# Kernel optimization log

Hardware: AMD Instinct MI355X
Metric: run time of the kernel (lower is better)

## Reference

```python
import jax, jax.numpy as jnp
import numpy as np

N_HEAD = 12

def setup_inputs() -> dict:
    key = jax.random.key(0)
    ks = jax.random.split(key, 3)
    B, T, D = 4, 2048, 768
    x = jax.random.normal(ks[0], (B, T, D), dtype=jnp.float32)
    W_qkv = jax.random.normal(ks[1], (D, 3 * D), dtype=jnp.float32) * (1.0 / np.sqrt(D))
    b_qkv = jnp.zeros((3 * D,), dtype=jnp.float32)
    W_o = jax.random.normal(ks[2], (D, D), dtype=jnp.float32) * (1.0 / np.sqrt(D))
    b_o = jnp.zeros((D,), dtype=jnp.float32)
    return {"x": x, "W_qkv": W_qkv, "b_qkv": b_qkv, "W_o": W_o, "b_o": b_o}


def reference(x, W_qkv, b_qkv, W_o, b_o):
    B, T, D = x.shape
    H = N_HEAD
    hd = D // H
    qkv = x @ W_qkv + b_qkv                      # [B,T,3D]
    q, k, v = jnp.split(qkv, 3, axis=-1)
    # [B,T,D] -> [B,H,T,hd]
    q = q.reshape(B, T, H, hd).transpose(0, 2, 1, 3)
    k = k.reshape(B, T, H, hd).transpose(0, 2, 1, 3)
    v = v.reshape(B, T, H, hd).transpose(0, 2, 1, 3)
    scale = 1.0 / np.sqrt(hd).astype(np.float32)
    scores = jnp.einsum('bhqd,bhkd->bhqk', q, k) * scale   # [B,H,T,T]
    causal = jnp.tril(jnp.ones((T, T), dtype=bool))
    scores = jnp.where(causal[None, None, :, :], scores, -jnp.inf)
    attn = jax.nn.softmax(scores, axis=-1)
    out = jnp.einsum('bhqk,bhkd->bhqd', attn, v)            # [B,H,T,hd]
    out = out.transpose(0, 2, 1, 3).reshape(B, T, D)
    return out @ W_o + b_o
```

## Files before the change

kernel.cpp:

```cpp
#include <hip/hip_runtime.h>
#include <hip/hip_bf16.h>

typedef __bf16 bf16_t;
typedef float f32x4 __attribute__((ext_vector_type(4)));
typedef bf16_t bf16x8 __attribute__((ext_vector_type(8)));
typedef bf16_t bf16x4 __attribute__((ext_vector_type(4)));

#define MFMA16(a, b, c) __builtin_amdgcn_mfma_f32_16x16x32_bf16(a, b, c, 0, 0, 0)

#define QSCALE 0.18033688011112042f

__device__ __forceinline__ void gl_lds16(const bf16_t* g, bf16_t* l) {
    __builtin_amdgcn_global_load_lds(
        (const __attribute__((address_space(1))) unsigned int*)g,
        (__attribute__((address_space(3))) unsigned int*)l, 16, 0, 0);
}

__device__ __forceinline__ float fexp2(float x) {
    float y;
    asm("v_exp_f32 %0, %1" : "=v"(y) : "v"(x));
    return y;
}

__global__ __launch_bounds__(256) void conv_x(const float* __restrict__ in,
                                              bf16_t* __restrict__ out, int n) {
    int i = (blockIdx.x * 256 + threadIdx.x) * 4;
    if (i >= n) return;
    float4 v = *(const float4*)(in + i);
    bf16x4 o = { (bf16_t)v.x, (bf16_t)v.y, (bf16_t)v.z, (bf16_t)v.w };
    *(bf16x4*)(out + i) = o;
}

__global__ __launch_bounds__(256) void conv_t(const float* __restrict__ in,
                                              bf16_t* __restrict__ out,
                                              int R, int C) {
    __shared__ float t[32][33];
    const int bx = blockIdx.x * 32;
    const int by = blockIdx.y * 32;
    const int tx = threadIdx.x & 31;
    const int ty = threadIdx.x >> 5;
#pragma unroll
    for (int i = 0; i < 4; i++)
        t[ty + i * 8][tx] = in[(size_t)(by + ty + i * 8) * C + bx + tx];
    __syncthreads();
#pragma unroll
    for (int i = 0; i < 4; i++)
        out[(size_t)(bx + ty + i * 8) * R + by + tx] = (bf16_t)t[tx][ty + i * 8];
}

__global__ __launch_bounds__(256) void vtrans(const bf16_t* __restrict__ Vp,
                                              bf16_t* __restrict__ Vt) {
    __shared__ __align__(16) bf16_t Ts[64 * 72];
    const int t0 = blockIdx.x * 64;
    const int bh = blockIdx.y;
    const int r  = threadIdx.x >> 2;
    const int cb = (threadIdx.x & 3) * 16;
    const bf16_t* src = Vp + (((size_t)bh * 2048 + t0 + r) << 6) + cb;
    *(bf16x8*)(Ts + r * 72 + cb)     = *(const bf16x8*)(src);
    *(bf16x8*)(Ts + r * 72 + cb + 8) = *(const bf16x8*)(src + 8);
    __syncthreads();
    const int f  = threadIdx.x >> 2;
    const int tb = (threadIdx.x & 3) * 16;
    bf16_t* dst = Vt + (((size_t)bh * 64 + f) << 11) + t0 + tb;
    bf16x8 a, b;
#pragma unroll
    for (int i = 0; i < 8; i++) a[i] = Ts[(tb + i) * 72 + f];
#pragma unroll
    for (int i = 0; i < 8; i++) b[i] = Ts[(tb + 8 + i) * 72 + f];
    *(bf16x8*)(dst)     = a;
    *(bf16x8*)(dst + 8) = b;
}

template <int EPI>
__global__ __launch_bounds__(256) void gemm_bt(
    const bf16_t* __restrict__ A, const bf16_t* __restrict__ Bt,
    const float* __restrict__ bias,
    void* __restrict__ O0v, bf16_t* __restrict__ O1, bf16_t* __restrict__ O2,
    int M, int N, int K)
{
    __shared__ __align__(16) bf16_t As[2][128 * 32];
    __shared__ __align__(16) bf16_t Bs[2][128 * 32];

    const int tid  = threadIdx.x;
    const int wid  = tid >> 6;
    const int lane = tid & 63;
    const int quad = lane >> 4;
    const int l15  = lane & 15;
    const int wm   = (wid >> 1) * 64;
    const int wn   = (wid & 1) * 64;

    const int mtiles = M >> 7;
    const int mtpx   = mtiles >> 3;
    const int bid    = blockIdx.x;
    const int xcd    = bid & 7;
    const int slot   = bid >> 3;
    const int m0     = (xcd * mtpx + (slot % mtpx)) << 7;
    const int n0     = (slot / mtpx) << 7;

    f32x4 acc[4][4];
#pragma unroll
    for (int i = 0; i < 4; i++)
#pragma unroll
        for (int j = 0; j < 4; j++) acc[i][j] = (f32x4){0.f, 0.f, 0.f, 0.f};

    const int srow = tid >> 2;
    const int scol = (tid & 3) * 8;
    const bf16_t* ag0 = A  + (size_t)(m0 + srow) * K + scol;
    const bf16_t* ag1 = A  + (size_t)(m0 + 64 + srow) * K + scol;
    const bf16_t* bg0 = Bt + (size_t)(n0 + srow) * K + scol;
    const bf16_t* bg1 = Bt + (size_t)(n0 + 64 + srow) * K + scol;

    auto prefetch = [&](int k0, int buf) {
        gl_lds16(ag0 + k0, As[buf] + tid * 8);
        gl_lds16(ag1 + k0, As[buf] + 2048 + tid * 8);
        gl_lds16(bg0 + k0, Bs[buf] + tid * 8);
        gl_lds16(bg1 + k0, Bs[buf] + 2048 + tid * 8);
    };

    const int niter = K >> 5;
    prefetch(0, 0);
    for (int i = 0; i < niter; i++) {
        __syncthreads();
        if (i + 1 < niter) prefetch((i + 1) << 5, (i + 1) & 1);
        const bf16_t* Ap = As[i & 1];
        const bf16_t* Bp = Bs[i & 1];

        bf16x8 af[4], bfr[4];
#pragma unroll
        for (int ii = 0; ii < 4; ii++)
            af[ii] = *(const bf16x8*)(Ap + (wm + ii * 16 + l15) * 32 + quad * 8);
#pragma unroll
        for (int j = 0; j < 4; j++)
            bfr[j] = *(const bf16x8*)(Bp + (wn + j * 16 + l15) * 32 + quad * 8);
#pragma unroll
        for (int ii = 0; ii < 4; ii++)
#pragma unroll
            for (int j = 0; j < 4; j++)
                acc[ii][j] = MFMA16(af[ii], bfr[j], acc[ii][j]);
    }

    if (EPI == 0) {
        const int sec = n0 / 768;
        const float scale = (sec == 0) ? QSCALE : 1.f;
        bf16_t* dst = (sec == 0) ? (bf16_t*)O0v : (sec == 1 ? O1 : O2);
#pragma unroll
        for (int i = 0; i < 4; i++) {
            const int mbase = m0 + wm + i * 16 + quad * 4;
#pragma unroll
            for (int j = 0; j < 4; j++) {
                const int n  = n0 + wn + j * 16 + l15;
                const float bv = bias[n];
                const int d    = n - sec * 768;
                const int h    = d >> 6;
                const int feat = d & 63;
#pragma unroll
                for (int r = 0; r < 4; r++) {
                    const int mm = mbase + r;
                    const int b  = mm >> 11;
                    const int tt = mm & 2047;
                    const int bh = b * 12 + h;
                    dst[(((size_t)bh * 2048 + tt) << 6) + feat] =
                        (bf16_t)((acc[i][j][r] + bv) * scale);
                }
            }
        }
    } else {
#pragma unroll
        for (int i = 0; i < 4; i++) {
            const int mbase = m0 + wm + i * 16 + quad * 4;
#pragma unroll
            for (int j = 0; j < 4; j++) {
                const int n  = n0 + wn + j * 16 + l15;
                const float bv = bias[n];
#pragma unroll
                for (int r = 0; r < 4; r++)
                    ((float*)O0v)[(size_t)(mbase + r) * N + n] = acc[i][j][r] + bv;
            }
        }
    }
}

__global__ __launch_bounds__(256) void attn_k(
    const bf16_t* __restrict__ Q, const bf16_t* __restrict__ Kb,
    const bf16_t* __restrict__ Vt,
    bf16_t* __restrict__ Op0, bf16_t* __restrict__ Op1,
    float* __restrict__ Lp0, float* __restrict__ Lp1)
{
    __shared__ __align__(16) bf16_t Ks[2 * 4096];
    __shared__ __align__(16) bf16_t Vs[2 * 4096];
    __shared__ __align__(16) bf16_t Ps[4 * 16 * 64];

    const int tid  = threadIdx.x;
    const int wid  = tid >> 6;
    const int lane = tid & 63;
    const int quad = lane >> 4;
    const int l15  = lane & 15;

    const int bid  = blockIdx.x;
    const int xcd  = bid & 7;
    const int slot = bid >> 3;
    const int bh   = xcd * 6 + (slot >> 5);
    const int px   = slot & 31;
    const int p    = px >> 1;
    const int hpar = px & 1;

    const bf16_t* Qb  = Q  + ((size_t)bh << 17);
    const bf16_t* Kbh = Kb + ((size_t)bh << 17);
    const bf16_t* Vbh = Vt + ((size_t)bh << 17);

    bf16_t* Pw = Ps + wid * 1024;
    const int swl = l15 & 7;
    bf16_t* pwr[4];
#pragma unroll
    for (int c = 0; c < 4; c++)
        pwr[c] = Pw + l15 * 64 + (((((c << 1) | (quad >> 1))) ^ swl) << 3) + ((quad & 1) << 2);
    const bf16_t* prd[2];
#pragma unroll
    for (int kk = 0; kk < 2; kk++)
        prd[kk] = Pw + l15 * 64 + ((((kk << 2) | quad) ^ swl) << 3);

    bf16_t* Op = hpar ? Op1 : Op0;
    float*  Lp = hpar ? Lp1 : Lp0;

    const bf16x8 ones = { (bf16_t)1.f, (bf16_t)1.f, (bf16_t)1.f, (bf16_t)1.f,
                          (bf16_t)1.f, (bf16_t)1.f, (bf16_t)1.f, (bf16_t)1.f };

    const int srow = tid >> 2;
    const int scol = (tid & 3) * 8;

    auto prefetch = [&](int j, int buf) {
        const int kv0 = j * 64;
        bf16_t* kd = Ks + buf * 4096 + tid * 8;
        bf16_t* vd = Vs + buf * 4096 + tid * 8;
#pragma unroll
        for (int c = 0; c < 2; c++) {
            gl_lds16(Kbh + (size_t)(kv0 + srow) * 64 + c * 32 + scol, kd + c * 2048);
            gl_lds16(Vbh + (size_t)srow * 2048 + kv0 + c * 32 + scol, vd + c * 2048);
        }
    };

#pragma unroll
    for (int half = 0; half < 2; half++) {
        const int qt = half == 0 ? (31 - p) : p;
        const int q0 = qt * 64;
        const int qg = q0 + wid * 16 + l15;

        bf16x8 qf[2];
        {
            const bf16_t* qp = Qb + ((size_t)qg << 6) + quad * 8;
            qf[0] = *(const bf16x8*)(qp);
            qf[1] = *(const bf16x8*)(qp + 32);
        }

        f32x4 lacc = (f32x4){0.f, 0.f, 0.f, 0.f};
        f32x4 oacc[4];
#pragma unroll
        for (int f = 0; f < 4; f++) oacc[f] = (f32x4){0.f, 0.f, 0.f, 0.f};

        const int cnt = (qt >= hpar) ? ((qt - hpar) >> 1) + 1 : 0;
        if (cnt > 0) prefetch(hpar, 0);

        for (int i = 0; i < cnt; i++) {
            const int j   = hpar + 2 * i;
            const int kv0 = j * 64;
            __syncthreads();
            if (i + 1 < cnt) prefetch(j + 2, (i + 1) & 1);
            const bf16_t* Kp = Ks + (i & 1) * 4096;
            const bf16_t* Vp = Vs + (i & 1) * 4096;

            f32x4 st[4];
#pragma unroll
            for (int c = 0; c < 4; c++) {
                st[c] = (f32x4){0.f, 0.f, 0.f, 0.f};
#pragma unroll
                for (int kk = 0; kk < 2; kk++) {
                    bf16x8 kf = *(const bf16x8*)(Kp + kk * 2048 + (c * 16 + l15) * 32 + quad * 8);
                    st[c] = MFMA16(kf, qf[kk], st[c]);
                }
            }

            if (j == qt) {
                const int kvb = kv0 + quad * 4;
#pragma unroll
                for (int c = 0; c < 4; c++)
#pragma unroll
                    for (int r = 0; r < 4; r++)
                        if (kvb + c * 16 + r > qg) st[c][r] = -3e38f;
            }

#pragma unroll
            for (int c = 0; c < 4; c++) {
                bf16x4 pk = { (bf16_t)fexp2(st[c][0]), (bf16_t)fexp2(st[c][1]),
                              (bf16_t)fexp2(st[c][2]), (bf16_t)fexp2(st[c][3]) };
                *(bf16x4*)pwr[c] = pk;
            }

            bf16x8 pb[2];
#pragma unroll
            for (int kk = 0; kk < 2; kk++)
                pb[kk] = *(const bf16x8*)prd[kk];

            lacc = MFMA16(ones, pb[0], lacc);
            lacc = MFMA16(ones, pb[1], lacc);

#pragma unroll
            for (int f = 0; f < 4; f++)
#pragma unroll
                for (int kk = 0; kk < 2; kk++) {
                    bf16x8 vf = *(const bf16x8*)(Vp + kk * 2048 + (f * 16 + l15) * 32 + quad * 8);
                    oacc[f] = MFMA16(vf, pb[kk], oacc[f]);
                }
        }
        __syncthreads();

        const size_t obase = (((size_t)bh * 2048 + qg) << 6) + quad * 4;
#pragma unroll
        for (int f = 0; f < 4; f++) {
            bf16x4 o = { (bf16_t)(oacc[f][0]), (bf16_t)(oacc[f][1]),
                         (bf16_t)(oacc[f][2]), (bf16_t)(oacc[f][3]) };
            *(bf16x4*)(Op + obase + f * 16) = o;
        }
        if (quad == 0) Lp[(size_t)bh * 2048 + qg] = lacc[0];
    }
}

__global__ __launch_bounds__(256) void comb_k(
    const bf16_t* __restrict__ Op0, const bf16_t* __restrict__ Op1,
    const float* __restrict__ Lp0, const float* __restrict__ Lp1,
    bf16_t* __restrict__ AO)
{
    const size_t e  = ((size_t)blockIdx.x * 256 + threadIdx.x) * 8;
    const int bh    = (int)(e >> 17);
    const int t     = (int)(e >> 6) & 2047;
    const int feat  = (int)e & 63;
    const int b     = bh / 12;
    const int h     = bh - b * 12;
    const float inv = 1.0f / (Lp0[(size_t)bh * 2048 + t] + Lp1[(size_t)bh * 2048 + t]);
    bf16x8 o0 = *(const bf16x8*)(Op0 + e);
    bf16x8 o1 = *(const bf16x8*)(Op1 + e);
    bf16x8 o;
#pragma unroll
    for (int k = 0; k < 8; k++)
        o[k] = (bf16_t)(((float)o0[k] + (float)o1[k]) * inv);
    *(bf16x8*)(AO + ((size_t)(b * 2048 + t) * 768 + h * 64 + feat)) = o;
}

extern "C" void kernel_launch(void* const* d_in, const int* in_sizes, int n_in,
                              void* d_out, int out_size, void* d_ws, size_t ws_size,
                              hipStream_t stream)
{
    const float* x    = (const float*)d_in[0];
    const float* Wqkv = (const float*)d_in[1];
    const float* bqkv = (const float*)d_in[2];
    const float* Wo   = (const float*)d_in[3];
    const float* bo   = (const float*)d_in[4];
    float* out = (float*)d_out;

    const size_t per = (size_t)48 * 2048 * 64;
    bf16_t* Qs  = (bf16_t*)d_ws;
    bf16_t* Kk  = Qs + per;
    bf16_t* Vt  = Kk + per;
    bf16_t* AO  = Vt + per;
    bf16_t* xb  = AO + per;
    bf16_t* Wt  = xb + per;
    bf16_t* Wot = Wt + (size_t)2304 * 768;
    float*  Lp0 = (float*)(Wot + (size_t)768 * 768);
    float*  Lp1 = Lp0 + (size_t)48 * 2048;
    bf16_t* Op0 = xb;
    bf16_t* Op1 = (bf16_t*)d_out;
    bf16_t* Vpl = (bf16_t*)d_out + per;

    conv_x<<<6144, 256, 0, stream>>>(x, xb, 8192 * 768);
    conv_t<<<dim3(72, 24), 256, 0, stream>>>(Wqkv, Wt, 768, 2304);
    conv_t<<<dim3(24, 24), 256, 0, stream>>>(Wo, Wot, 768, 768);

    gemm_bt<0><<<18 * 64, 256, 0, stream>>>(
        xb, Wt, bqkv, (void*)Qs, Kk, Vpl, 8192, 2304, 768);
    vtrans<<<dim3(32, 48), 256, 0, stream>>>(Vpl, Vt);
    attn_k<<<1536, 256, 0, stream>>>(Qs, Kk, Vt, Op0, Op1, Lp0, Lp1);
    comb_k<<<3072, 256, 0, stream>>>(Op0, Op1, Lp0, Lp1, AO);
    gemm_bt<1><<<6 * 64, 256, 0, stream>>>(
        AO, Wot, bo, (void*)out, nullptr, nullptr, 8192, 768, 768);
}
```

Baseline: 219.6 us.

## Drop KV-split in attention, normalize in-kernel, and merge prep conversion kernels

The attention kernel stops splitting the KV range across two blocks by parity. Each block now walks all KV tiles for its paired query tiles and writes normalized output straight into the [B,T,D] layout, so the combine kernel and the partial-output and row-sum buffers go away. The three fp32-to-bf16 conversion kernels are merged into one launch. The cost is half as many attention blocks (768 instead of 1536), each with twice the serial work, which lowers parallelism on the GPU in exchange for less memory traffic and fewer launches.

New measurement: 205.0 us. 6.7% less time.

```diff
diff --git a/kernel.cpp b/kernel.cpp
--- a/kernel.cpp
+++ b/kernel.cpp
@@ -22,21 +22,10 @@
     return y;
 }
 
-__global__ __launch_bounds__(256) void conv_x(const float* __restrict__ in,
-                                              bf16_t* __restrict__ out, int n) {
-    int i = (blockIdx.x * 256 + threadIdx.x) * 4;
-    if (i >= n) return;
-    float4 v = *(const float4*)(in + i);
-    bf16x4 o = { (bf16_t)v.x, (bf16_t)v.y, (bf16_t)v.z, (bf16_t)v.w };
-    *(bf16x4*)(out + i) = o;
-}
-
-__global__ __launch_bounds__(256) void conv_t(const float* __restrict__ in,
-                                              bf16_t* __restrict__ out,
-                                              int R, int C) {
-    __shared__ float t[32][33];
-    const int bx = blockIdx.x * 32;
-    const int by = blockIdx.y * 32;
+__device__ __forceinline__ void conv_t_body(const float* __restrict__ in,
+                                            bf16_t* __restrict__ out,
+                                            int R, int C, int bx, int by,
+                                            float (*t)[33]) {
     const int tx = threadIdx.x & 31;
     const int ty = threadIdx.x >> 5;
 #pragma unroll
@@ -46,6 +35,27 @@
 #pragma unroll
     for (int i = 0; i < 4; i++)
         out[(size_t)(bx + ty + i * 8) * R + by + tx] = (bf16_t)t[tx][ty + i * 8];
+}
+
+__global__ __launch_bounds__(256) void prep_k(
+    const float* __restrict__ x,    bf16_t* __restrict__ xb,
+    const float* __restrict__ Wqkv, bf16_t* __restrict__ Wt,
+    const float* __restrict__ Wo,   bf16_t* __restrict__ Wot)
+{
+    __shared__ float t[32][33];
+    const int blk = blockIdx.x;
+    if (blk < 6144) {
+        const int i = (blk * 256 + threadIdx.x) * 4;
+        float4 v = *(const float4*)(x + i);
+        bf16x4 o = { (bf16_t)v.x, (bf16_t)v.y, (bf16_t)v.z, (bf16_t)v.w };
+        *(bf16x4*)(xb + i) = o;
+    } else if (blk < 7872) {
+        const int idx = blk - 6144;
+        conv_t_body(Wqkv, Wt, 768, 2304, (idx % 72) * 32, (idx / 72) * 32, t);
+    } else {
+        const int idx = blk - 7872;
+        conv_t_body(Wo, Wot, 768, 768, (idx % 24) * 32, (idx / 24) * 32, t);
+    }
 }
 
 __global__ __launch_bounds__(256) void vtrans(const bf16_t* __restrict__ Vp,
@@ -182,9 +192,7 @@
 
 __global__ __launch_bounds__(256) void attn_k(
     const bf16_t* __restrict__ Q, const bf16_t* __restrict__ Kb,
-    const bf16_t* __restrict__ Vt,
-    bf16_t* __restrict__ Op0, bf16_t* __restrict__ Op1,
-    float* __restrict__ Lp0, float* __restrict__ Lp1)
+    const bf16_t* __restrict__ Vt, bf16_t* __restrict__ AO)
 {
     __shared__ __align__(16) bf16_t Ks[2 * 4096];
     __shared__ __align__(16) bf16_t Vs[2 * 4096];
@@ -199,10 +207,8 @@
     const int bid  = blockIdx.x;
     const int xcd  = bid & 7;
     const int slot = bid >> 3;
-    const int bh   = xcd * 6 + (slot >> 5);
-    const int px   = slot & 31;
-    const int p    = px >> 1;
-    const int hpar = px & 1;
+    const int bh   = xcd * 6 + (slot >> 4);
+    const int p    = slot & 15;
 
     const bf16_t* Qb  = Q  + ((size_t)bh << 17);
     const bf16_t* Kbh = Kb + ((size_t)bh << 17);
@@ -218,9 +224,6 @@
 #pragma unroll
     for (int kk = 0; kk < 2; kk++)
         prd[kk] = Pw + l15 * 64 + ((((kk << 2) | quad) ^ swl) << 3);
-
-    bf16_t* Op = hpar ? Op1 : Op0;
-    float*  Lp = hpar ? Lp1 : Lp0;
 
     const bf16x8 ones = { (bf16_t)1.f, (bf16_t)1.f, (bf16_t)1.f, (bf16_t)1.f,
                           (bf16_t)1.f, (bf16_t)1.f, (bf16_t)1.f, (bf16_t)1.f };
@@ -238,6 +241,9 @@
             gl_lds16(Vbh + (size_t)srow * 2048 + kv0 + c * 32 + scol, vd + c * 2048);
         }
     };
+
+    const int b = bh / 12;
+    const int h = bh - b * 12;
 
 #pragma unroll
     for (int half = 0; half < 2; half++) {
@@ -257,14 +263,12 @@
 #pragma unroll
         for (int f = 0; f < 4; f++) oacc[f] = (f32x4){0.f, 0.f, 0.f, 0.f};
 
-        const int cnt = (qt >= hpar) ? ((qt - hpar) >> 1) + 1 : 0;
-        if (cnt > 0) prefetch(hpar, 0);
+        const int cnt = qt + 1;
+        prefetch(0, 0);
 
         for (int i = 0; i < cnt; i++) {
-            const int j   = hpar + 2 * i;
-            const int kv0 = j * 64;
             __syncthreads();
-            if (i + 1 < cnt) prefetch(j + 2, (i + 1) & 1);
+            if (i + 1 < cnt) prefetch(i + 1, (i + 1) & 1);
             const bf16_t* Kp = Ks + (i & 1) * 4096;
             const bf16_t* Vp = Vs + (i & 1) * 4096;
 
@@ -279,8 +283,8 @@
                 }
             }
 
-            if (j == qt) {
-                const int kvb = kv0 + quad * 4;
+            if (i == qt) {
+                const int kvb = q0 + quad * 4;
 #pragma unroll
                 for (int c = 0; c < 4; c++)
 #pragma unroll
@@ -313,36 +317,15 @@
         }
         __syncthreads();
 
-        const size_t obase = (((size_t)bh * 2048 + qg) << 6) + quad * 4;
+        const float inv = 1.0f / lacc[0];
+        bf16_t* dst = AO + ((size_t)(b * 2048 + qg)) * 768 + h * 64 + quad * 4;
 #pragma unroll
         for (int f = 0; f < 4; f++) {
-            bf16x4 o = { (bf16_t)(oacc[f][0]), (bf16_t)(oacc[f][1]),
-                         (bf16_t)(oacc[f][2]), (bf16_t)(oacc[f][3]) };
-            *(bf16x4*)(Op + obase + f * 16) = o;
-        }
-        if (quad == 0) Lp[(size_t)bh * 2048 + qg] = lacc[0];
+            bf16x4 o = { (bf16_t)(oacc[f][0] * inv), (bf16_t)(oacc[f][1] * inv),
+                         (bf16_t)(oacc[f][2] * inv), (bf16_t)(oacc[f][3] * inv) };
+            *(bf16x4*)(dst + f * 16) = o;
+        }
     }
-}
-
-__global__ __launch_bounds__(256) void comb_k(
-    const bf16_t* __restrict__ Op0, const bf16_t* __restrict__ Op1,
-    const float* __restrict__ Lp0, const float* __restrict__ Lp1,
-    bf16_t* __restrict__ AO)
-{
-    const size_t e  = ((size_t)blockIdx.x * 256 + threadIdx.x) * 8;
-    const int bh    = (int)(e >> 17);
-    const int t     = (int)(e >> 6) & 2047;
-    const int feat  = (int)e & 63;
-    const int b     = bh / 12;
-    const int h     = bh - b * 12;
-    const float inv = 1.0f / (Lp0[(size_t)bh * 2048 + t] + Lp1[(size_t)bh * 2048 + t]);
-    bf16x8 o0 = *(const bf16x8*)(Op0 + e);
-    bf16x8 o1 = *(const bf16x8*)(Op1 + e);
-    bf16x8 o;
-#pragma unroll
-    for (int k = 0; k < 8; k++)
-        o[k] = (bf16_t)(((float)o0[k] + (float)o1[k]) * inv);
-    *(bf16x8*)(AO + ((size_t)(b * 2048 + t) * 768 + h * 64 + feat)) = o;
 }
 
 extern "C" void kernel_launch(void* const* d_in, const int* in_sizes, int n_in,
@@ -364,21 +347,14 @@
     bf16_t* xb  = AO + per;
     bf16_t* Wt  = xb + per;
     bf16_t* Wot = Wt + (size_t)2304 * 768;
-    float*  Lp0 = (float*)(Wot + (size_t)768 * 768);
-    float*  Lp1 = Lp0 + (size_t)48 * 2048;
-    bf16_t* Op0 = xb;
-    bf16_t* Op1 = (bf16_t*)d_out;
-    bf16_t* Vpl = (bf16_t*)d_out + per;
-
-    conv_x<<<6144, 256, 0, stream>>>(x, xb, 8192 * 768);
-    conv_t<<<dim3(72, 24), 256, 0, stream>>>(Wqkv, Wt, 768, 2304);
-    conv_t<<<dim3(24, 24), 256, 0, stream>>>(Wo, Wot, 768, 768);
+    bf16_t* Vpl = (bf16_t*)d_out;
+
+    prep_k<<<8448, 256, 0, stream>>>(x, xb, Wqkv, Wt, Wo, Wot);
 
     gemm_bt<0><<<18 * 64, 256, 0, stream>>>(
         xb, Wt, bqkv, (void*)Qs, Kk, Vpl, 8192, 2304, 768);
     vtrans<<<dim3(32, 48), 256, 0, stream>>>(Vpl, Vt);
-    attn_k<<<1536, 256, 0, stream>>>(Qs, Kk, Vt, Op0, Op1, Lp0, Lp1);
-    comb_k<<<3072, 256, 0, stream>>>(Op0, Op1, Lp0, Lp1, AO);
+    attn_k<<<768, 256, 0, stream>>>(Qs, Kk, Vt, AO);
     gemm_bt<1><<<6 * 64, 256, 0, stream>>>(
         AO, Wot, bo, (void*)out, nullptr, nullptr, 8192, 768, 768);
 }
```
